# Kernel tuning notes

Hardware: AMD Instinct MI355X
Metric: run time of the kernel (lower is better)

The kernel has to match this reference:

```python
import jax, jax.numpy as jnp
import numpy as np
from jax import lax

N_ANCHOR = 9
FEAT_STRIDE = 16
N_PRE_NMS = 2000
N_POST_NMS = 300
NMS_THRESH = 0.7
MIN_SIZE = 16.0
SCALE = 1.0


def generate_anchor(feat_stride, h, w):
    # base anchors: scales {8,16,32} x ratios {0.5,1,2}, (y1,x1,y2,x2)
    base = float(feat_stride)
    ratios = jnp.array([0.5, 1.0, 2.0], jnp.float32)
    scales = jnp.array([8.0, 16.0, 32.0], jnp.float32)
    py = px = base / 2.0
    hs = base * scales[None, :] * jnp.sqrt(ratios)[:, None]          # [3,3]
    ws = base * scales[None, :] * jnp.sqrt(1.0 / ratios)[:, None]    # [3,3]
    anchor_base = jnp.stack([py - hs / 2, px - ws / 2, py + hs / 2, px + ws / 2], axis=-1).reshape(9, 4)
    shift_y = jnp.arange(h, dtype=jnp.float32) * feat_stride
    shift_x = jnp.arange(w, dtype=jnp.float32) * feat_stride
    sy, sx = jnp.meshgrid(shift_y, shift_x, indexing='ij')
    shifts = jnp.stack([sy, sx, sy, sx], axis=-1).reshape(-1, 1, 4)  # [h*w,1,4]
    return (shifts + anchor_base[None]).reshape(-1, 4)               # [h*w*9,4]


def loc2bbox(anchor, loc):
    ah = anchor[:, 2] - anchor[:, 0]
    aw = anchor[:, 3] - anchor[:, 1]
    acy = anchor[:, 0] + 0.5 * ah
    acx = anchor[:, 1] + 0.5 * aw
    dy, dx, dh, dw = loc[:, 0], loc[:, 1], loc[:, 2], loc[:, 3]
    cy = dy * ah + acy
    cx = dx * aw + acx
    h = jnp.exp(dh) * ah
    w = jnp.exp(dw) * aw
    return jnp.stack([cy - 0.5 * h, cx - 0.5 * w, cy + 0.5 * h, cx + 0.5 * w], axis=1)


def nms_keep(boxes, thresh):
    # boxes sorted by descending score; returns keep mask
    y1, x1, y2, x2 = boxes[:, 0], boxes[:, 1], boxes[:, 2], boxes[:, 3]
    area = (y2 - y1) * (x2 - x1)
    yy1 = jnp.maximum(y1[:, None], y1[None, :])
    xx1 = jnp.maximum(x1[:, None], x1[None, :])
    yy2 = jnp.minimum(y2[:, None], y2[None, :])
    xx2 = jnp.minimum(x2[:, None], x2[None, :])
    inter = jnp.clip(yy2 - yy1, 0.0) * jnp.clip(xx2 - xx1, 0.0)
    iou = inter / (area[:, None] + area[None, :] - inter + 1e-9)
    n = boxes.shape[0]

    def step(supp, i):
        keep_i = jnp.logical_not(supp[i])
        supp = supp | (keep_i & (iou[i] > thresh))
        return supp, keep_i

    _, keep = lax.scan(step, jnp.zeros((n,), bool), jnp.arange(n))
    return keep


def proposal_single(loc, score, anchor, img_h, img_w):
    roi = loc2bbox(anchor, loc)
    roi = jnp.stack([
        jnp.clip(roi[:, 0], 0.0, img_h),
        jnp.clip(roi[:, 1], 0.0, img_w),
        jnp.clip(roi[:, 2], 0.0, img_h),
        jnp.clip(roi[:, 3], 0.0, img_w)], axis=1)
    hs = roi[:, 2] - roi[:, 0]
    ws = roi[:, 3] - roi[:, 1]
    ms = MIN_SIZE * SCALE
    score = jnp.where((hs >= ms) & (ws >= ms), score, -jnp.inf)
    top_s, idx = lax.top_k(score, N_PRE_NMS)
    boxes = roi[idx]
    keep = nms_keep(boxes, NMS_THRESH) & jnp.isfinite(top_s)
    order = jnp.argsort(jnp.logical_not(keep), stable=True)[:N_POST_NMS]
    out = boxes[order]
    kout = keep[order]
    return jnp.where(kout[:, None], out, 0.0), kout


def _conv(x, w, b, pad):
    y = lax.conv_general_dilated(x, w, (1, 1), pad, dimension_numbers=('NCHW', 'OIHW', 'NCHW'))
    return y + b[None, :, None, None]


def setup_inputs() -> dict:
    key = jax.random.key(0)
    ks = jax.random.split(key, 7)
    n, c, h, w = 8, 512, 64, 64
    x = jax.random.normal(ks[0], (n, c, h, w), jnp.float32)
    conv_w = 0.01 * jax.random.normal(ks[1], (512, c, 3, 3), jnp.float32)
    conv_b = 0.01 * jax.random.normal(ks[2], (512,), jnp.float32)
    score_w = 0.01 * jax.random.normal(ks[3], (2 * N_ANCHOR, 512, 1, 1), jnp.float32)
    score_b = 0.01 * jax.random.normal(ks[4], (2 * N_ANCHOR,), jnp.float32)
    params_w = 0.01 * jax.random.normal(ks[5], (4 * N_ANCHOR, 512, 1, 1), jnp.float32)
    params_b = 0.01 * jax.random.normal(ks[6], (4 * N_ANCHOR,), jnp.float32)
    return {"x": x, "conv_w": conv_w, "conv_b": conv_b, "score_w": score_w, "score_b": score_b,
            "params_w": params_w, "params_b": params_b, "img_h": 1024, "img_w": 1024}


def reference(x, conv_w, conv_b, score_w, score_b, params_w, params_b, img_h, img_w):
    n, _, h, w = x.shape
    anchor = generate_anchor(FEAT_STRIDE, h, w)                       # [h*w*9,4]
    mid = jax.nn.relu(_conv(x, conv_w, conv_b, 'SAME'))               # [n,512,h,w]
    rpn_params = _conv(mid, params_w, params_b, 'VALID')              # [n,36,h,w]
    rpn_params = rpn_params.transpose(0, 2, 3, 1).reshape(n, -1, 4)   # [n,h*w*9,4]
    rpn_score = _conv(mid, score_w, score_b, 'VALID')                 # [n,18,h,w]
    rpn_score = rpn_score.transpose(0, 2, 3, 1).reshape(n, -1, 2)     # [n,h*w*9,2]
    fg_score = jax.nn.softmax(rpn_score, axis=2)[:, :, 1]             # [n,h*w*9]
    rois, keep = jax.vmap(lambda l, s: proposal_single(l, s, anchor, float(img_h), float(img_w)))(rpn_params, fg_score)
    roi_index = jnp.repeat(jnp.arange(n, dtype=jnp.int32), N_POST_NMS)
    rois = rois.reshape(-1, 4)
    return rpn_params, rpn_score, rois, roi_index, anchor


if __name__ == '__main__':
    out = reference(**setup_inputs())
    print([o.shape for o in out])
```

## Files before the change

kernel.cpp:

```cpp
#include <hip/hip_runtime.h>
#include <math.h>

typedef _Float16 f16x8 __attribute__((ext_vector_type(8)));
typedef float f32x4 __attribute__((ext_vector_type(4)));
typedef unsigned long long u64;

#define OUT_PARAMS 0L
#define OUT_SCORE  1179648L
#define OUT_ROIS   1769472L
#define OUT_IDX    1779072L
#define OUT_ANCH   1781472L

#define WS_WT2   0L
#define WS_W2H   27648L
#define WS_W2L   1207296L
#define WS_X2    2386944L
#define WS_MID   20229120L
#define WS_FG    2386944L
#define WS_KEYS  2681856L
#define WS_BOX   2976768L
#define WS_SELK  4156416L
#define WS_SBOX  4172800L
#define WS_SUPP  4238336L

__global__ void k_transpose_w(const float* __restrict__ conv_w,
                              const float* __restrict__ score_w,
                              const float* __restrict__ params_w,
                              _Float16* __restrict__ W2h, _Float16* __restrict__ W2l,
                              float* __restrict__ wt2) {
  int e = blockIdx.x * 256 + threadIdx.x;
  if (e < 9 * 512 * 512) {
    int tap = e >> 18, rem = e & 262143;
    int oc = rem >> 9, c = rem & 511;
    float v = conv_w[(oc * 512 + c) * 9 + tap] * 1024.0f;
    _Float16 h = (_Float16)v;
    W2h[e] = h;
    W2l[e] = (_Float16)(v - (float)h);
  }
  if (e < 512 * 54) {
    int o = e % 54, c = e / 54;
    wt2[e] = (o < 18) ? score_w[o * 512 + c] : params_w[(o - 18) * 512 + c];
  }
}

__global__ void k_zero_pad(_Float16* __restrict__ X2) {
  const int t = blockIdx.x * 256 + threadIdx.x;
  if (t >= 8 * 260 * 128) return;
  const int s8 = t & 127;
  const int px_i = (t >> 7) % 260;
  const int n = (t >> 7) / 260;
  int prow, pcol;
  if (px_i < 66) { prow = 0; pcol = px_i; }
  else if (px_i < 132) { prow = 65; pcol = px_i - 66; }
  else if (px_i < 196) { prow = px_i - 132 + 1; pcol = 0; }
  else { prow = px_i - 196 + 1; pcol = 65; }
  _Float16* dst = X2 + (((size_t)(n * 66 + prow) * 66) + pcol) * 1024 + s8 * 8;
  float4 z = {0.f, 0.f, 0.f, 0.f};
  *(float4*)dst = z;
}

__global__ __launch_bounds__(256) void k_split_x(const float* __restrict__ x,
                                                 _Float16* __restrict__ X2) {
  __shared__ float t[64][67];
  const int pxb = blockIdx.x;
  const int c0  = blockIdx.y * 64;
  const int n   = blockIdx.z;
  const int tid = threadIdx.x;
  const int a = tid >> 6, b = tid & 63;
#pragma unroll
  for (int i = 0; i < 16; ++i) {
    int c_l = i * 4 + a;
    t[c_l][b] = x[((size_t)(n * 512 + c0 + c_l) * 4096) + pxb * 64 + b];
  }
  __syncthreads();
#pragma unroll
  for (int it = 0; it < 2; ++it) {
    const int w = it * 256 + tid;
    const int px_l = w >> 3, cg8 = w & 7;
    f16x8 hv, lv;
#pragma unroll
    for (int j = 0; j < 8; ++j) {
      const float fs = t[cg8 * 8 + j][px_l] * 512.0f;
      const _Float16 h = (_Float16)fs;
      hv[j] = h;
      lv[j] = (_Float16)(fs - (float)h);
    }
    const int c = c0 + cg8 * 8;
    const int cb = c >> 5, cloc = c & 31;
    _Float16* base = X2 + (((size_t)(n * 66 + pxb + 1) * 66) + px_l + 1) * 1024 + cb * 64;
    *(f16x8*)(base + cloc) = hv;
    *(f16x8*)(base + 32 + cloc) = lv;
  }
}

__global__ __launch_bounds__(256, 2) void k_conv_mfma(
    const _Float16* __restrict__ X2,
    const _Float16* __restrict__ W2h, const _Float16* __restrict__ W2l,
    const float* __restrict__ bias, float* __restrict__ mid) {
  __shared__ _Float16 XH[8448];
  __shared__ _Float16 XL[8448];

  const int n   = blockIdx.x >> 5;
  const int rp  = blockIdx.x & 31;
  const int oc0 = blockIdx.y * 128;
  const int tid = threadIdx.x;
  const int lane = tid & 63, wid = tid >> 6;
  const int wm = wid >> 1, wn = wid & 1;
  const int l15 = lane & 15, kg = lane >> 4;

  f32x4 acch[4][4], accl[4][4];
#pragma unroll
  for (int i = 0; i < 4; ++i)
#pragma unroll
    for (int j = 0; j < 4; ++j) {
      acch[i][j] = (f32x4){0.f, 0.f, 0.f, 0.f};
      accl[i][j] = (f32x4){0.f, 0.f, 0.f, 0.f};
    }

  for (int cb = 0; cb < 16; ++cb) {
    __syncthreads();
    for (int u = tid; u < 1056; u += 256) {
      const int px = u >> 2, sd = u & 3;
      const int cg = sd ^ ((px >> 1) & 3);
      const int hrow = px / 66, hcol = px - hrow * 66;
      const _Float16* base = X2 +
          (((size_t)(n * 66 + rp * 2 + hrow) * 66) + hcol) * 1024 + cb * 64;
      const f16x8 hv = *(const f16x8*)(base + cg * 8);
      const f16x8 lv = *(const f16x8*)(base + 32 + cg * 8);
      *(f16x8*)(XH + u * 8) = hv;
      *(f16x8*)(XL + u * 8) = lv;
    }
    __syncthreads();

#pragma unroll
    for (int ky = 0; ky < 3; ++ky) {
#pragma unroll
      for (int kx = 0; kx < 3; ++kx) {
        const int tap = ky * 3 + kx;
        f16x8 ah[4], al[4], bh[4], bl[4];
#pragma unroll
        for (int mf = 0; mf < 4; ++mf) {
          const size_t aoff =
              ((size_t)(tap * 512 + oc0 + wm * 64 + mf * 16 + l15)) * 512 + cb * 32 + kg * 8;
          ah[mf] = *(const f16x8*)(W2h + aoff);
          al[mf] = *(const f16x8*)(W2l + aoff);
        }
#pragma unroll
        for (int nf = 0; nf < 4; ++nf) {
          const int lpx = (wn + ky) * 66 + nf * 16 + l15 + kx;
          const int off = lpx * 32 + ((kg ^ ((lpx >> 1) & 3)) * 8);
          bh[nf] = *(const f16x8*)(&XH[off]);
          bl[nf] = *(const f16x8*)(&XL[off]);
        }
#pragma unroll
        for (int mf = 0; mf < 4; ++mf)
#pragma unroll
          for (int nf = 0; nf < 4; ++nf) {
            acch[mf][nf] = __builtin_amdgcn_mfma_f32_16x16x32_f16(ah[mf], bh[nf], acch[mf][nf], 0, 0, 0);
            accl[mf][nf] = __builtin_amdgcn_mfma_f32_16x16x32_f16(ah[mf], bl[nf], accl[mf][nf], 0, 0, 0);
            accl[mf][nf] = __builtin_amdgcn_mfma_f32_16x16x32_f16(al[mf], bh[nf], accl[mf][nf], 0, 0, 0);
          }
      }
    }
  }

  const float inv = 1.0f / (1024.0f * 512.0f);
  const int y = rp * 2 + wn;
#pragma unroll
  for (int mf = 0; mf < 4; ++mf) {
#pragma unroll
    for (int r = 0; r < 4; ++r) {
      const int oc = oc0 + wm * 64 + mf * 16 + kg * 4 + r;
      const float bv = bias[oc];
      float* mp = mid + (((size_t)(n * 512 + oc) * 64 + y) * 64);
#pragma unroll
      for (int nf = 0; nf < 4; ++nf) {
        const int xcol = nf * 16 + l15;
        mp[xcol] = fmaxf((acch[mf][nf][r] + accl[mf][nf][r]) * inv + bv, 0.f);
      }
    }
  }
}

__global__ __launch_bounds__(256) void k_1x1(
    const float* __restrict__ mid, const float* __restrict__ wt2,
    const float* __restrict__ score_b, const float* __restrict__ params_b,
    float* __restrict__ out, float* __restrict__ fg) {
  const int t = blockIdx.x * 256 + threadIdx.x;
  const int half = t & 1;
  const int p = t >> 1;
  const int n = p >> 12, hw = p & 4095;
  float acc[54];
#pragma unroll
  for (int o = 0; o < 54; ++o) acc[o] = 0.f;
  const float* m = mid + (size_t)n * 2097152 + (size_t)half * 256 * 4096 + hw;
  const float* wt = wt2 + half * 256 * 54;
  for (int c = 0; c < 256; ++c) {
    const float mv = m[(size_t)c * 4096];
    const float* w = wt + c * 54;
#pragma unroll
    for (int o = 0; o < 54; ++o) acc[o] = fmaf(w[o], mv, acc[o]);
  }
#pragma unroll
  for (int o = 0; o < 54; ++o) acc[o] += __shfl_xor(acc[o], 1);
  if (half) return;
#pragma unroll
  for (int o = 0; o < 18; ++o) acc[o] += score_b[o];
#pragma unroll
  for (int o = 0; o < 36; ++o) acc[18 + o] += params_b[o];

  float* so = out + OUT_SCORE + (size_t)n * 73728 + (size_t)hw * 18;
#pragma unroll
  for (int o = 0; o < 18; ++o) so[o] = acc[o];
  float* po = out + OUT_PARAMS + (size_t)n * 147456 + (size_t)hw * 36;
#pragma unroll
  for (int o = 0; o < 36; ++o) po[o] = acc[18 + o];
  float* f = fg + (size_t)n * 36864 + hw * 9;
#pragma unroll
  for (int a = 0; a < 9; ++a) {
    float d = acc[a * 2 + 1] - acc[a * 2 + 0];
    f[a] = 1.f / (1.f + expf(-d));
  }
}

__global__ void k_proposals(const float* __restrict__ out_params,
                            const float* __restrict__ fg,
                            const int* __restrict__ ih_p, const int* __restrict__ iw_p,
                            float* __restrict__ boxes, unsigned int* __restrict__ keys,
                            float* __restrict__ anchor_out) {
  const int g = blockIdx.x * 256 + threadIdx.x;
  if (g >= 8 * 36864) return;
  const int n = g / 36864, i = g % 36864;
  const int hw = i / 9, a = i % 9;
  const float ih = (float)ih_p[0], iw = (float)iw_p[0];
  const float ratios[3] = {0.5f, 1.f, 2.f};
  const float scales[3] = {8.f, 16.f, 32.f};
  const float rr = ratios[a / 3], sc = scales[a % 3];
  const float hs = (16.f * sc) * sqrtf(rr);
  const float ws_ = (16.f * sc) * sqrtf(1.f / rr);
  const float sy = (float)((hw >> 6) * 16);
  const float sx = (float)((hw & 63) * 16);
  const float ay1 = sy + (8.f - hs * 0.5f), ax1 = sx + (8.f - ws_ * 0.5f);
  const float ay2 = sy + (8.f + hs * 0.5f), ax2 = sx + (8.f + ws_ * 0.5f);
  if (n == 0) {
    float4 av; av.x = ay1; av.y = ax1; av.z = ay2; av.w = ax2;
    *(float4*)&anchor_out[(size_t)i * 4] = av;
  }
  const float ah = ay2 - ay1, aw = ax2 - ax1;
  const float acy = ay1 + 0.5f * ah, acx = ax1 + 0.5f * aw;
  const float* loc = out_params + (size_t)n * 147456 + (size_t)i * 4;
  const float dy = loc[0], dx = loc[1], dh = loc[2], dw = loc[3];
  const float cy = dy * ah + acy, cx = dx * aw + acx;
  const float h = expf(dh) * ah, w = expf(dw) * aw;
  const float y1 = fminf(fmaxf(cy - 0.5f * h, 0.f), ih);
  const float x1 = fminf(fmaxf(cx - 0.5f * w, 0.f), iw);
  const float y2 = fminf(fmaxf(cy + 0.5f * h, 0.f), ih);
  const float x2 = fminf(fmaxf(cx + 0.5f * w, 0.f), iw);
  float4 bx; bx.x = y1; bx.y = x1; bx.z = y2; bx.w = x2;
  *(float4*)&boxes[(size_t)g * 4] = bx;
  float s = fg[g];
  if (!((y2 - y1) >= 16.f && (x2 - x1) >= 16.f)) s = -INFINITY;
  const unsigned int b = __float_as_uint(s);
  keys[g] = (b & 0x80000000u) ? ~b : (b | 0x80000000u);
}

__global__ __launch_bounds__(1024) void k_select(
    const unsigned int* __restrict__ keys, const float* __restrict__ boxes,
    unsigned int* __restrict__ selkey, float* __restrict__ sboxes) {
  __shared__ unsigned int hist[16][256];
  __shared__ unsigned long long sel[4096];
  __shared__ unsigned int s_prefix, s_remk, s_cnt;
  const int n = blockIdx.x, tid = threadIdx.x;
  const int lane = tid & 63;
  const unsigned int* kk = keys + (size_t)n * 36864;
  if (tid == 0) { s_prefix = 0; s_remk = 2000; s_cnt = 0; }
  const int hslot = tid >> 6;

  for (int byte = 3; byte >= 0; --byte) {
    for (int b2 = tid; b2 < 4096; b2 += 1024) ((unsigned int*)hist)[b2] = 0;
    __syncthreads();
    const unsigned pfx = s_prefix;
    const unsigned hmask = (byte == 3) ? 0u : (0xFFFFFFFFu << ((byte + 1) * 8));
    for (int i2 = tid; i2 < 36864; i2 += 1024) {
      const unsigned k = kk[i2];
      if ((k & hmask) == (pfx & hmask)) {
        const unsigned b8 = (k >> (byte * 8)) & 255u;
        unsigned long long peers = __ballot(1);
#pragma unroll
        for (int bit = 0; bit < 8; ++bit) {
          const unsigned long long bb = __ballot((b8 >> bit) & 1u);
          peers &= ((b8 >> bit) & 1u) ? bb : ~bb;
        }
        peers &= __ballot(1);
        if (lane == __builtin_ctzll(peers))
          atomicAdd(&hist[hslot][b8], (unsigned)__popcll(peers));
      }
    }
    __syncthreads();
    if (tid < 256) {
      unsigned s2 = 0;
#pragma unroll
      for (int j = 0; j < 16; ++j) s2 += hist[j][tid];
      hist[0][tid] = s2;
    }
    __syncthreads();
    if (tid == 0) {
      unsigned rem = s_remk;
      int b2 = 255;
      for (;; --b2) {
        const unsigned c2 = hist[0][b2];
        if (c2 >= rem) break;
        rem -= c2;
      }
      s_prefix = pfx | ((unsigned)b2 << (byte * 8));
      s_remk = rem;
    }
    __syncthreads();
  }
  const unsigned T = s_prefix;

  for (int i2 = tid; i2 < 36864; i2 += 1024) {
    const unsigned k = kk[i2];
    if (k >= T) {
      const unsigned long long m = __ballot(1);
      const int ldr = __builtin_ctzll(m);
      unsigned basep = 0;
      if (lane == ldr) basep = atomicAdd(&s_cnt, (unsigned)__popcll(m));
      basep = __shfl(basep, ldr);
      const unsigned p2 = basep + (unsigned)__popcll(m & ((1ull << lane) - 1ull));
      if (p2 < 4096)
        sel[p2] = ((unsigned long long)k << 32) | (unsigned)(~i2);
    }
  }
  __syncthreads();
  unsigned cnt = s_cnt; if (cnt > 4096) cnt = 4096;
  for (int i2 = (int)cnt + tid; i2 < 4096; i2 += 1024) sel[i2] = 0ull;

  for (int k2 = 2; k2 <= 4096; k2 <<= 1) {
    for (int j = k2 >> 1; j > 0; j >>= 1) {
      __syncthreads();
      for (int t = tid; t < 2048; t += 1024) {
        const int i1 = (t << 1) - (t & (j - 1));
        const int i2 = i1 + j;
        const unsigned long long va = sel[i1], vb = sel[i2];
        const bool sw = ((i1 & k2) == 0) ? (va < vb) : (va > vb);
        if (sw) { sel[i1] = vb; sel[i2] = va; }
      }
    }
  }
  __syncthreads();

  for (int s2 = tid; s2 < 2048; s2 += 1024) {
    const unsigned long long comp = sel[s2];
    unsigned key = (unsigned)(comp >> 32);
    unsigned idx = ~(unsigned)(comp & 0xFFFFFFFFu);
    float4 bx; bx.x = 0.f; bx.y = 0.f; bx.z = 0.f; bx.w = 0.f;
    if (comp != 0ull) bx = *(const float4*)&boxes[((size_t)n * 36864 + idx) * 4];
    else key = 0;
    selkey[n * 2048 + s2] = key;
    *(float4*)&sboxes[((size_t)n * 2048 + s2) * 4] = bx;
  }
}

__global__ void k_nms_matrix(const float* __restrict__ sboxes,
                             unsigned long long* __restrict__ supp) {
  const int t = blockIdx.x * 256 + threadIdx.x;
  if (t >= 8 * 2000 * 32) return;
  const int n = t / 64000, rem = t % 64000;
  const int i = rem >> 5, w = rem & 31;
  const float4 bi = *(const float4*)&sboxes[((size_t)n * 2048 + i) * 4];
  const float areai = (bi.z - bi.x) * (bi.w - bi.y);
  unsigned long long bits = 0ull;
  const int j0 = w * 64;
  for (int jj = 0; jj < 64; ++jj) {
    const int j = j0 + jj;
    if (j >= 2000) break;
    const float4 bj = *(const float4*)&sboxes[((size_t)n * 2048 + j) * 4];
    const float areaj = (bj.z - bj.x) * (bj.w - bj.y);
    const float yy1 = fmaxf(bi.x, bj.x), xx1 = fmaxf(bi.y, bj.y);
    const float yy2 = fminf(bi.z, bj.z), xx2 = fminf(bi.w, bj.w);
    const float ih2 = fmaxf(yy2 - yy1, 0.f), iw2 = fmaxf(xx2 - xx1, 0.f);
    const float inter = ih2 * iw2;
    const float iou = inter / (areai + areaj - inter + 1e-9f);
    if (iou > 0.7f) bits |= (1ull << jj);
  }
  supp[((size_t)n * 2000 + i) * 32 + w] = bits;
}

__global__ void k_nms_scan(const unsigned long long* __restrict__ supp,
                           const unsigned int* __restrict__ selkey,
                           const float* __restrict__ sboxes,
                           float* __restrict__ out) {
  const int n = blockIdx.x;
  const int lane = threadIdx.x;
  const unsigned long long* sp = supp + (size_t)n * 64000;
  const bool ld = lane < 32;
  unsigned long long removed = 0ull, keepmask = 0ull;
#define LDROW(i) (ld ? sp[(size_t)(i) * 32 + lane] : 0ull)
  unsigned long long r0 = LDROW(0), r1 = LDROW(1), r2 = LDROW(2), r3 = LDROW(3),
                     r4 = LDROW(4), r5 = LDROW(5), r6 = LDROW(6), r7 = LDROW(7);
  for (int g = 0; g < 250; ++g) {
    unsigned long long n0 = 0, n1 = 0, n2 = 0, n3 = 0, n4 = 0, n5 = 0, n6 = 0, n7 = 0;
    if (g < 249) {
      const int nb = (g + 1) * 8;
      n0 = LDROW(nb); n1 = LDROW(nb + 1); n2 = LDROW(nb + 2); n3 = LDROW(nb + 3);
      n4 = LDROW(nb + 4); n5 = LDROW(nb + 5); n6 = LDROW(nb + 6); n7 = LDROW(nb + 7);
    }
#define STEP(K, RK)                                                       \
    {                                                                     \
      const int i = g * 8 + K;                                            \
      const unsigned long long remw = __shfl(removed, i >> 6);            \
      if (!((remw >> (i & 63)) & 1ull)) {                                 \
        if (ld) removed |= RK;                                            \
        if (lane == (i >> 6)) keepmask |= (1ull << (i & 63));             \
      }                                                                   \
    }
    STEP(0, r0) STEP(1, r1) STEP(2, r2) STEP(3, r3)
    STEP(4, r4) STEP(5, r5) STEP(6, r6) STEP(7, r7)
#undef STEP
    r0 = n0; r1 = n1; r2 = n2; r3 = n3; r4 = n4; r5 = n5; r6 = n6; r7 = n7;
  }
#undef LDROW
  int running = 0;
  for (int ci = 0; ci < 32; ++ci) {
    const unsigned long long km = __shfl(keepmask, ci);
    const int i = ci * 64 + lane;
    const unsigned key = selkey[n * 2048 + i];
    const bool fin = (key >= 0x80000000u);
    const bool kf = (((km >> lane) & 1ull) != 0ull) && fin;
    const unsigned long long ball = __ballot(kf);
    const int rank = running + __popcll(ball & ((1ull << lane) - 1ull));
    if (kf && rank < 300) {
      const float4 bx = *(const float4*)&sboxes[((size_t)n * 2048 + i) * 4];
      *(float4*)&out[OUT_ROIS + ((size_t)n * 300 + rank) * 4] = bx;
    }
    running += __popcll(ball);
  }
  const int kept = running < 300 ? running : 300;
  for (int r2 = kept + lane; r2 < 300; r2 += 64) {
    float4 z; z.x = 0.f; z.y = 0.f; z.z = 0.f; z.w = 0.f;
    *(float4*)&out[OUT_ROIS + ((size_t)n * 300 + r2) * 4] = z;
  }
  for (int r2 = lane; r2 < 300; r2 += 64)
    out[OUT_IDX + n * 300 + r2] = (float)n;
}

extern "C" void kernel_launch(void* const* d_in, const int* in_sizes, int n_in,
                              void* d_out, int out_size, void* d_ws, size_t ws_size,
                              hipStream_t stream) {
  const float* x        = (const float*)d_in[0];
  const float* conv_w   = (const float*)d_in[1];
  const float* conv_b   = (const float*)d_in[2];
  const float* score_w  = (const float*)d_in[3];
  const float* score_b  = (const float*)d_in[4];
  const float* params_w = (const float*)d_in[5];
  const float* params_b = (const float*)d_in[6];
  const int*   ih       = (const int*)d_in[7];
  const int*   iw       = (const int*)d_in[8];
  float* out = (float*)d_out;
  float* ws  = (float*)d_ws;

  float* wt2 = ws + WS_WT2;
  _Float16* W2h = (_Float16*)(ws + WS_W2H);
  _Float16* W2l = (_Float16*)(ws + WS_W2L);
  _Float16* X2  = (_Float16*)(ws + WS_X2);
  float* mid = ws + WS_MID;
  float* fg  = ws + WS_FG;
  unsigned int* keys = (unsigned int*)(ws + WS_KEYS);
  float* boxes = ws + WS_BOX;
  unsigned int* selkey = (unsigned int*)(ws + WS_SELK);
  float* sboxes = ws + WS_SBOX;
  u64* supp = (u64*)(ws + WS_SUPP);

  hipLaunchKernelGGL(k_transpose_w, dim3(9216), dim3(256), 0, stream,
                     conv_w, score_w, params_w, W2h, W2l, wt2);
  hipLaunchKernelGGL(k_zero_pad, dim3(1040), dim3(256), 0, stream, X2);
  hipLaunchKernelGGL(k_split_x, dim3(64, 8, 8), dim3(256), 0, stream, x, X2);
  hipLaunchKernelGGL(k_conv_mfma, dim3(256, 4), dim3(256), 0, stream,
                     X2, W2h, W2l, conv_b, mid);
  hipLaunchKernelGGL(k_1x1, dim3(256), dim3(256), 0, stream,
                     mid, wt2, score_b, params_b, out, fg);
  hipLaunchKernelGGL(k_proposals, dim3(1152), dim3(256), 0, stream,
                     out + OUT_PARAMS, fg, ih, iw, boxes, keys, out + OUT_ANCH);
  hipLaunchKernelGGL(k_select, dim3(8), dim3(1024), 0, stream,
                     keys, boxes, selkey, sboxes);
  hipLaunchKernelGGL(k_nms_matrix, dim3(2000), dim3(256), 0, stream,
                     sboxes, supp);
  hipLaunchKernelGGL(k_nms_scan, dim3(8), dim3(64), 0, stream,
                     supp, selkey, sboxes, out);
}
```

Measured before the change: 1.348 ms.

## Fuse proposal decoding into 1x1 kernel and stage two channel blocks per sync

The separate proposal kernel is folded into the 1x1 head kernel, which now decodes boxes, anchors and sort keys directly from its register accumulators. This removes one launch and the round trip of the fg and params buffers. The conv kernel now loads two channel blocks into doubled shared memory per barrier pair, halving the number of syncs, and raises wave priority around the MFMA section. The larger LDS footprint (about 66KB per block) may reduce occupancy below the requested two blocks per CU, and the fused epilogue adds register pressure to k_1x1.

```diff
diff --git a/kernel.cpp b/kernel.cpp
--- a/kernel.cpp
+++ b/kernel.cpp
@@ -16,7 +16,6 @@
 #define WS_W2L   1207296L
 #define WS_X2    2386944L
 #define WS_MID   20229120L
-#define WS_FG    2386944L
 #define WS_KEYS  2681856L
 #define WS_BOX   2976768L
 #define WS_SELK  4156416L
@@ -97,8 +96,8 @@
     const _Float16* __restrict__ X2,
     const _Float16* __restrict__ W2h, const _Float16* __restrict__ W2l,
     const float* __restrict__ bias, float* __restrict__ mid) {
-  __shared__ _Float16 XH[8448];
-  __shared__ _Float16 XL[8448];
+  __shared__ _Float16 XH[2][8448];
+  __shared__ _Float16 XL[2][8448];
 
   const int n   = blockIdx.x >> 5;
   const int rp  = blockIdx.x & 31;
@@ -117,51 +116,59 @@
       accl[i][j] = (f32x4){0.f, 0.f, 0.f, 0.f};
     }
 
-  for (int cb = 0; cb < 16; ++cb) {
-    __syncthreads();
-    for (int u = tid; u < 1056; u += 256) {
-      const int px = u >> 2, sd = u & 3;
+  for (int cbp = 0; cbp < 8; ++cbp) {
+    __syncthreads();
+    for (int u = tid; u < 2112; u += 256) {
+      const int h = (u >= 1056) ? 1 : 0;
+      const int v = u - h * 1056;
+      const int px = v >> 2, sd = v & 3;
       const int cg = sd ^ ((px >> 1) & 3);
       const int hrow = px / 66, hcol = px - hrow * 66;
       const _Float16* base = X2 +
-          (((size_t)(n * 66 + rp * 2 + hrow) * 66) + hcol) * 1024 + cb * 64;
+          (((size_t)(n * 66 + rp * 2 + hrow) * 66) + hcol) * 1024 + (cbp * 2 + h) * 64;
       const f16x8 hv = *(const f16x8*)(base + cg * 8);
       const f16x8 lv = *(const f16x8*)(base + 32 + cg * 8);
-      *(f16x8*)(XH + u * 8) = hv;
-      *(f16x8*)(XL + u * 8) = lv;
-    }
-    __syncthreads();
-
-#pragma unroll
-    for (int ky = 0; ky < 3; ++ky) {
-#pragma unroll
-      for (int kx = 0; kx < 3; ++kx) {
-        const int tap = ky * 3 + kx;
-        f16x8 ah[4], al[4], bh[4], bl[4];
-#pragma unroll
-        for (int mf = 0; mf < 4; ++mf) {
-          const size_t aoff =
-              ((size_t)(tap * 512 + oc0 + wm * 64 + mf * 16 + l15)) * 512 + cb * 32 + kg * 8;
-          ah[mf] = *(const f16x8*)(W2h + aoff);
-          al[mf] = *(const f16x8*)(W2l + aoff);
+      *(f16x8*)(&XH[h][v * 8]) = hv;
+      *(f16x8*)(&XL[h][v * 8]) = lv;
+    }
+    __syncthreads();
+
+    __builtin_amdgcn_s_setprio(1);
+#pragma unroll
+    for (int hh = 0; hh < 2; ++hh) {
+      const int cb = cbp * 2 + hh;
+#pragma unroll
+      for (int ky = 0; ky < 3; ++ky) {
+#pragma unroll
+        for (int kx = 0; kx < 3; ++kx) {
+          const int tap = ky * 3 + kx;
+          f16x8 ah[4], al[4], bh[4], bl[4];
+#pragma unroll
+          for (int mf = 0; mf < 4; ++mf) {
+            const size_t aoff =
+                ((size_t)(tap * 512 + oc0 + wm * 64 + mf * 16 + l15)) * 512 + cb * 32 + kg * 8;
+            ah[mf] = *(const f16x8*)(W2h + aoff);
+            al[mf] = *(const f16x8*)(W2l + aoff);
+          }
+#pragma unroll
+          for (int nf = 0; nf < 4; ++nf) {
+            const int lpx = (wn + ky) * 66 + nf * 16 + l15 + kx;
+            const int off = lpx * 32 + ((kg ^ ((lpx >> 1) & 3)) * 8);
+            bh[nf] = *(const f16x8*)(&XH[hh][off]);
+            bl[nf] = *(const f16x8*)(&XL[hh][off]);
+          }
+#pragma unroll
+          for (int mf = 0; mf < 4; ++mf)
+#pragma unroll
+            for (int nf = 0; nf < 4; ++nf) {
+              acch[mf][nf] = __builtin_amdgcn_mfma_f32_16x16x32_f16(ah[mf], bh[nf], acch[mf][nf], 0, 0, 0);
+              accl[mf][nf] = __builtin_amdgcn_mfma_f32_16x16x32_f16(ah[mf], bl[nf], accl[mf][nf], 0, 0, 0);
+              accl[mf][nf] = __builtin_amdgcn_mfma_f32_16x16x32_f16(al[mf], bh[nf], accl[mf][nf], 0, 0, 0);
+            }
         }
-#pragma unroll
-        for (int nf = 0; nf < 4; ++nf) {
-          const int lpx = (wn + ky) * 66 + nf * 16 + l15 + kx;
-          const int off = lpx * 32 + ((kg ^ ((lpx >> 1) & 3)) * 8);
-          bh[nf] = *(const f16x8*)(&XH[off]);
-          bl[nf] = *(const f16x8*)(&XL[off]);
-        }
-#pragma unroll
-        for (int mf = 0; mf < 4; ++mf)
-#pragma unroll
-          for (int nf = 0; nf < 4; ++nf) {
-            acch[mf][nf] = __builtin_amdgcn_mfma_f32_16x16x32_f16(ah[mf], bh[nf], acch[mf][nf], 0, 0, 0);
-            accl[mf][nf] = __builtin_amdgcn_mfma_f32_16x16x32_f16(ah[mf], bl[nf], accl[mf][nf], 0, 0, 0);
-            accl[mf][nf] = __builtin_amdgcn_mfma_f32_16x16x32_f16(al[mf], bh[nf], accl[mf][nf], 0, 0, 0);
-          }
       }
     }
+    __builtin_amdgcn_s_setprio(0);
   }
 
   const float inv = 1.0f / (1024.0f * 512.0f);
@@ -185,7 +192,9 @@
 __global__ __launch_bounds__(256) void k_1x1(
     const float* __restrict__ mid, const float* __restrict__ wt2,
     const float* __restrict__ score_b, const float* __restrict__ params_b,
-    float* __restrict__ out, float* __restrict__ fg) {
+    const int* __restrict__ ih_p, const int* __restrict__ iw_p,
+    float* __restrict__ out, float* __restrict__ boxes,
+    unsigned int* __restrict__ keys) {
   const int t = blockIdx.x * 256 + threadIdx.x;
   const int half = t & 1;
   const int p = t >> 1;
@@ -215,53 +224,43 @@
   float* po = out + OUT_PARAMS + (size_t)n * 147456 + (size_t)hw * 36;
 #pragma unroll
   for (int o = 0; o < 36; ++o) po[o] = acc[18 + o];
-  float* f = fg + (size_t)n * 36864 + hw * 9;
-#pragma unroll
-  for (int a = 0; a < 9; ++a) {
-    float d = acc[a * 2 + 1] - acc[a * 2 + 0];
-    f[a] = 1.f / (1.f + expf(-d));
-  }
-}
-
-__global__ void k_proposals(const float* __restrict__ out_params,
-                            const float* __restrict__ fg,
-                            const int* __restrict__ ih_p, const int* __restrict__ iw_p,
-                            float* __restrict__ boxes, unsigned int* __restrict__ keys,
-                            float* __restrict__ anchor_out) {
-  const int g = blockIdx.x * 256 + threadIdx.x;
-  if (g >= 8 * 36864) return;
-  const int n = g / 36864, i = g % 36864;
-  const int hw = i / 9, a = i % 9;
+
   const float ih = (float)ih_p[0], iw = (float)iw_p[0];
   const float ratios[3] = {0.5f, 1.f, 2.f};
   const float scales[3] = {8.f, 16.f, 32.f};
-  const float rr = ratios[a / 3], sc = scales[a % 3];
-  const float hs = (16.f * sc) * sqrtf(rr);
-  const float ws_ = (16.f * sc) * sqrtf(1.f / rr);
   const float sy = (float)((hw >> 6) * 16);
   const float sx = (float)((hw & 63) * 16);
-  const float ay1 = sy + (8.f - hs * 0.5f), ax1 = sx + (8.f - ws_ * 0.5f);
-  const float ay2 = sy + (8.f + hs * 0.5f), ax2 = sx + (8.f + ws_ * 0.5f);
-  if (n == 0) {
-    float4 av; av.x = ay1; av.y = ax1; av.z = ay2; av.w = ax2;
-    *(float4*)&anchor_out[(size_t)i * 4] = av;
-  }
-  const float ah = ay2 - ay1, aw = ax2 - ax1;
-  const float acy = ay1 + 0.5f * ah, acx = ax1 + 0.5f * aw;
-  const float* loc = out_params + (size_t)n * 147456 + (size_t)i * 4;
-  const float dy = loc[0], dx = loc[1], dh = loc[2], dw = loc[3];
-  const float cy = dy * ah + acy, cx = dx * aw + acx;
-  const float h = expf(dh) * ah, w = expf(dw) * aw;
-  const float y1 = fminf(fmaxf(cy - 0.5f * h, 0.f), ih);
-  const float x1 = fminf(fmaxf(cx - 0.5f * w, 0.f), iw);
-  const float y2 = fminf(fmaxf(cy + 0.5f * h, 0.f), ih);
-  const float x2 = fminf(fmaxf(cx + 0.5f * w, 0.f), iw);
-  float4 bx; bx.x = y1; bx.y = x1; bx.z = y2; bx.w = x2;
-  *(float4*)&boxes[(size_t)g * 4] = bx;
-  float s = fg[g];
-  if (!((y2 - y1) >= 16.f && (x2 - x1) >= 16.f)) s = -INFINITY;
-  const unsigned int b = __float_as_uint(s);
-  keys[g] = (b & 0x80000000u) ? ~b : (b | 0x80000000u);
+#pragma unroll
+  for (int a = 0; a < 9; ++a) {
+    const float rr = ratios[a / 3], sc = scales[a % 3];
+    const float hs = (16.f * sc) * sqrtf(rr);
+    const float ws_ = (16.f * sc) * sqrtf(1.f / rr);
+    const float ay1 = sy + (8.f - hs * 0.5f), ax1 = sx + (8.f - ws_ * 0.5f);
+    const float ay2 = sy + (8.f + hs * 0.5f), ax2 = sx + (8.f + ws_ * 0.5f);
+    const int i = hw * 9 + a;
+    if (n == 0) {
+      float4 av; av.x = ay1; av.y = ax1; av.z = ay2; av.w = ax2;
+      *(float4*)&out[OUT_ANCH + (size_t)i * 4] = av;
+    }
+    const float ah = ay2 - ay1, aw = ax2 - ax1;
+    const float acy = ay1 + 0.5f * ah, acx = ax1 + 0.5f * aw;
+    const float dy = acc[18 + a * 4 + 0], dx = acc[18 + a * 4 + 1];
+    const float dh = acc[18 + a * 4 + 2], dw = acc[18 + a * 4 + 3];
+    const float cy = dy * ah + acy, cx = dx * aw + acx;
+    const float h = expf(dh) * ah, w = expf(dw) * aw;
+    const float y1 = fminf(fmaxf(cy - 0.5f * h, 0.f), ih);
+    const float x1 = fminf(fmaxf(cx - 0.5f * w, 0.f), iw);
+    const float y2 = fminf(fmaxf(cy + 0.5f * h, 0.f), ih);
+    const float x2 = fminf(fmaxf(cx + 0.5f * w, 0.f), iw);
+    const int g = n * 36864 + i;
+    float4 bx; bx.x = y1; bx.y = x1; bx.z = y2; bx.w = x2;
+    *(float4*)&boxes[(size_t)g * 4] = bx;
+    const float d = acc[a * 2 + 1] - acc[a * 2 + 0];
+    float s = 1.f / (1.f + expf(-d));
+    if (!((y2 - y1) >= 16.f && (x2 - x1) >= 16.f)) s = -INFINITY;
+    const unsigned int b = __float_as_uint(s);
+    keys[g] = (b & 0x80000000u) ? ~b : (b | 0x80000000u);
+  }
 }
 
 __global__ __launch_bounds__(1024) void k_select(
@@ -465,7 +464,6 @@
   _Float16* W2l = (_Float16*)(ws + WS_W2L);
   _Float16* X2  = (_Float16*)(ws + WS_X2);
   float* mid = ws + WS_MID;
-  float* fg  = ws + WS_FG;
   unsigned int* keys = (unsigned int*)(ws + WS_KEYS);
   float* boxes = ws + WS_BOX;
   unsigned int* selkey = (unsigned int*)(ws + WS_SELK);
@@ -479,9 +477,7 @@
   hipLaunchKernelGGL(k_conv_mfma, dim3(256, 4), dim3(256), 0, stream,
                      X2, W2h, W2l, conv_b, mid);
   hipLaunchKernelGGL(k_1x1, dim3(256), dim3(256), 0, stream,
-                     mid, wt2, score_b, params_b, out, fg);
-  hipLaunchKernelGGL(k_proposals, dim3(1152), dim3(256), 0, stream,
-                     out + OUT_PARAMS, fg, ih, iw, boxes, keys, out + OUT_ANCH);
+                     mid, wt2, score_b, params_b, ih, iw, out, boxes, keys);
   hipLaunchKernelGGL(k_select, dim3(8), dim3(1024), 0, stream,
                      keys, boxes, selkey, sboxes);
   hipLaunchKernelGGL(k_nms_matrix, dim3(2000), dim3(256), 0, stream,
```

Measured after the change: 1.776 ms. 1.32x slower.
